# Performance work log

Hardware: AMD Instinct MI355X
Metric: run time of the kernel (lower is better)

Reference implementation:

```python
import jax, jax.numpy as jnp
import numpy as np

N = 50000   # n_nodes
E = 500000  # n_edges
D = 128     # input_dim == hidden_dim
L = 2       # n_layers
K = 5       # Chebyshev filter size


def setup_inputs() -> dict:
    key = jax.random.key(0)
    k0, k1, k2, k3, k4 = jax.random.split(key, 5)
    scale = 1.0 / np.sqrt(D)
    return {
        "edge_index": jax.random.randint(k0, (2, E), 0, N),
        "edge_weight": jax.random.uniform(k1, (E,), dtype=jnp.float32),
        "emb": jax.random.uniform(k2, (N, D), dtype=jnp.float32, minval=-1.0, maxval=1.0),
        "Wx": jax.random.normal(k3, (L, 3, K, D, D), dtype=jnp.float32) * scale,
        "bx": jnp.zeros((L, 3, D), dtype=jnp.float32),
        "Wh": jax.random.normal(k4, (L, 3, K, D, D), dtype=jnp.float32) * scale,
        "bh": jnp.zeros((L, 3, D), dtype=jnp.float32),
    }


def reference(edge_index, edge_weight, emb, Wx, bx, Wh, bh):
    src, dst = edge_index[0], edge_index[1]
    # ChebConv sym-normalized scaled Laplacian with lambda_max=2:
    # L_hat = L - I = -D^{-1/2} A D^{-1/2} (zero diagonal)
    deg = jax.ops.segment_sum(edge_weight, src, num_segments=N)
    dinv = jnp.where(deg > 0, deg ** -0.5, 0.0)
    w = -dinv[src] * edge_weight * dinv[dst]  # [E]

    def prop(x):  # L_hat @ x via gather/scatter over edges
        return jax.ops.segment_sum(w[:, None] * x[src], dst, num_segments=N)

    def cheb(x, W, b):  # sum_k T_k(L_hat) x W_k + b
        Tx0 = x
        out = Tx0 @ W[0]
        Tx1 = prop(Tx0)
        out = out + Tx1 @ W[1]
        for k in range(2, K):
            Tx2 = 2.0 * prop(Tx1) - Tx0
            out = out + Tx2 @ W[k]
            Tx0, Tx1 = Tx1, Tx2
        return out + b

    x = emb
    hidden_states = []
    for l in range(L):
        H = jnp.ones((N, D), x.dtype)  # init__hidd: ones
        Z = jax.nn.sigmoid(cheb(x, Wx[l, 0], bx[l, 0]) + cheb(H, Wh[l, 0], bh[l, 0]))
        R = jax.nn.sigmoid(cheb(x, Wx[l, 1], bx[l, 1]) + cheb(H, Wh[l, 1], bh[l, 1]))
        Ht = jnp.tanh(cheb(x, Wx[l, 2], bx[l, 2]) + cheb(H * R, Wh[l, 2], bh[l, 2]))
        Hn = Z * H + (1.0 - Z) * Ht
        h = jax.nn.relu(Hn)  # dropout is identity in eval mode
        hidden_states.append(h)
        x = h
    return x  # == hidden_states[-1]
```

## Files before the change

kernel.cpp:

```cpp
#include <hip/hip_runtime.h>
#include <math.h>

#define NN 50000
#define EE 500000
#define DD 128
#define KK 5
#define LL 2

typedef _Float16 f16x8 __attribute__((ext_vector_type(8)));
typedef float f32x4 __attribute__((ext_vector_type(4)));

__device__ __forceinline__ ushort f2h(float x) {
    union { _Float16 h; ushort u; } v; v.h = (_Float16)x; return v.u;
}


__global__ __launch_bounds__(256) void edge_pass1(
    const int* __restrict__ src, const int* __restrict__ dst,
    const float* __restrict__ ew,
    float* __restrict__ deg, int* __restrict__ hist)
{
    int e = blockIdx.x * blockDim.x + threadIdx.x;
    if (e >= EE) return;
    atomicAdd(&deg[src[e]], ew[e]);
    atomicAdd(&hist[dst[e]], 1);
}

__global__ __launch_bounds__(256) void dinv_kernel(
    const float* __restrict__ deg, float* __restrict__ dinv)
{
    int i = blockIdx.x * blockDim.x + threadIdx.x;
    if (i >= NN) return;
    float d = deg[i];
    dinv[i] = (d > 0.f) ? (1.f / sqrtf(d)) : 0.f;
}

__global__ __launch_bounds__(1024) void scan_kernel(
    const int* __restrict__ hist, int* __restrict__ row_ptr)
{
    __shared__ int buf[1024];
    __shared__ int carry;
    int tid = threadIdx.x;
    if (tid == 0) { carry = 0; row_ptr[0] = 0; }
    __syncthreads();
    for (int base = 0; base < NN; base += 1024) {
        int i = base + tid;
        int v = (i < NN) ? hist[i] : 0;
        buf[tid] = v;
        __syncthreads();
        for (int off = 1; off < 1024; off <<= 1) {
            int t = (tid >= off) ? buf[tid - off] : 0;
            __syncthreads();
            buf[tid] += t;
            __syncthreads();
        }
        int incl = buf[tid] + carry;
        if (i < NN) row_ptr[i + 1] = incl;
        __syncthreads();
        if (tid == 1023) carry = incl;
        __syncthreads();
    }
}

__global__ __launch_bounds__(256) void copy_fill(
    const int* __restrict__ row_ptr, int* __restrict__ fill)
{
    int i = blockIdx.x * blockDim.x + threadIdx.x;
    if (i < NN) fill[i] = row_ptr[i];
}

__global__ __launch_bounds__(256) void edge_scatter(
    const int* __restrict__ src, const int* __restrict__ dst,
    const float* __restrict__ ew, const float* __restrict__ dinv,
    int* __restrict__ fill,
    int* __restrict__ src_srt, float* __restrict__ w_srt)
{
    int e = blockIdx.x * blockDim.x + threadIdx.x;
    if (e >= EE) return;
    int s = src[e], t = dst[e];
    float w = -dinv[s] * ew[e] * dinv[t];
    int pos = atomicAdd(&fill[t], 1);
    src_srt[pos] = s;
    w_srt[pos] = w;
}

__global__ __launch_bounds__(256) void propv_kernel(
    const int* __restrict__ rp, const int* __restrict__ ss, const float* __restrict__ sw,
    const float* __restrict__ tin, const float* __restrict__ tprev, float* __restrict__ tout,
    float alpha, float beta, int ones_in, int ones_prev)
{
    int i = blockIdx.x * blockDim.x + threadIdx.x;
    if (i >= NN) return;
    float acc = 0.f;
    int e0 = rp[i], e1 = rp[i + 1];
    int e = e0;
    for (; e + 4 <= e1; e += 4) {
        float t0 = ones_in ? 1.f : tin[ss[e]];
        float t1v = ones_in ? 1.f : tin[ss[e + 1]];
        float t2v = ones_in ? 1.f : tin[ss[e + 2]];
        float t3v = ones_in ? 1.f : tin[ss[e + 3]];
        acc += sw[e] * t0 + sw[e + 1] * t1v + sw[e + 2] * t2v + sw[e + 3] * t3v;
    }
    for (; e < e1; ++e) {
        float tv = ones_in ? 1.f : tin[ss[e]];
        acc += sw[e] * tv;
    }
    float pv = ones_prev ? 1.f : (tprev ? tprev[i] : 0.f);
    tout[i] = alpha * acc + beta * pv;
}

__global__ __launch_bounds__(128) void colsum_kernel(
    const float* __restrict__ Wh, float* __restrict__ scol)
{
    int b = blockIdx.x;
    int k = b % KK;
    int g = (b / KK) % 2;
    int l = b / (2 * KK);
    int d = threadIdx.x;
    const float* Wp = Wh + ((size_t)((l * 3 + g) * KK + k)) * DD * DD;
    float s = 0.f;
    for (int r = 0; r < DD; ++r) s += Wp[r * DD + d];
    scol[((size_t)((l * 2 + g) * KK + k)) * DD + d] = s;
}

__global__ __launch_bounds__(256) void wconv_f16(
    const float* __restrict__ W, ushort* __restrict__ out, int mode)
{
    int t = blockIdx.x;
    int st = (mode == 0) ? t : ((t / KK) * 3 + 2) * KK + (t % KK);
    const float* Wp = W + (size_t)st * DD * DD;
    ushort* op = out + (size_t)t * DD * DD;
    for (int idx = threadIdx.x; idx < DD * DD; idx += 256) {
        int rb = idx >> 7, c = idx & 127;
        float w = Wp[c * DD + rb];
        int byte = rb * 256 + (((c * 2) ^ ((rb & 7) << 4)));
        *(ushort*)((char*)op + byte) = f2h(w);
    }
}

__global__ __launch_bounds__(256) void f32_to_f16(
    const float* __restrict__ in, ushort* __restrict__ out, int n8)
{
    int i = blockIdx.x * blockDim.x + threadIdx.x;
    if (i >= n8) return;
    float4 a = ((const float4*)in)[i * 2];
    float4 b = ((const float4*)in)[i * 2 + 1];
    f16x8 o;
    o[0] = (_Float16)a.x; o[1] = (_Float16)a.y; o[2] = (_Float16)a.z; o[3] = (_Float16)a.w;
    o[4] = (_Float16)b.x; o[5] = (_Float16)b.y; o[6] = (_Float16)b.z; o[7] = (_Float16)b.w;
    ((f16x8*)out)[i] = o;
}

__global__ __launch_bounds__(256) void prop_mat(
    const int* __restrict__ rp, const int* __restrict__ ss, const float* __restrict__ sw,
    const ushort* __restrict__ x, const ushort* __restrict__ prev,
    ushort* __restrict__ out, float alpha, float beta)
{
    int node = blockIdx.x * 16 + (threadIdx.x >> 4);
    if (node >= NN) return;
    int lane = threadIdx.x & 15;
    int c = lane * 8;
    float acc[8];
#pragma unroll
    for (int j = 0; j < 8; ++j) acc[j] = 0.f;
    int e0 = rp[node], e1 = rp[node + 1];
    int e = e0;
    for (; e + 4 <= e1; e += 4) {
        int s0 = ss[e], s1 = ss[e + 1], s2 = ss[e + 2], s3 = ss[e + 3];
        float w0 = sw[e], w1 = sw[e + 1], w2 = sw[e + 2], w3 = sw[e + 3];
        f16x8 r0 = *(const f16x8*)(x + (size_t)s0 * DD + c);
        f16x8 r1 = *(const f16x8*)(x + (size_t)s1 * DD + c);
        f16x8 r2 = *(const f16x8*)(x + (size_t)s2 * DD + c);
        f16x8 r3 = *(const f16x8*)(x + (size_t)s3 * DD + c);
#pragma unroll
        for (int j = 0; j < 8; ++j)
            acc[j] += w0 * (float)r0[j] + w1 * (float)r1[j] + w2 * (float)r2[j] + w3 * (float)r3[j];
    }
    for (; e < e1; ++e) {
        int s = ss[e];
        float w = sw[e];
        f16x8 r = *(const f16x8*)(x + (size_t)s * DD + c);
#pragma unroll
        for (int j = 0; j < 8; ++j) acc[j] += w * (float)r[j];
    }
    f16x8 o;
    if (beta != 0.f && prev) {
        f16x8 pv = *(const f16x8*)(prev + (size_t)node * DD + c);
#pragma unroll
        for (int j = 0; j < 8; ++j) o[j] = (_Float16)(alpha * acc[j] + beta * (float)pv[j]);
    } else {
#pragma unroll
        for (int j = 0; j < 8; ++j) o[j] = (_Float16)(alpha * acc[j]);
    }
    *(f16x8*)(out + (size_t)node * DD + c) = o;
}

__global__ __launch_bounds__(256) void cheb_mm_mfma(
    const ushort* __restrict__ T0, const ushort* __restrict__ T1,
    const ushort* __restrict__ T2, const ushort* __restrict__ T3,
    const ushort* __restrict__ T4,
    const ushort* __restrict__ Wt, int gate_stride,
    float* __restrict__ outbase, size_t out_stride, int accumulate, int ngates)
{
    __shared__ ushort Bs[DD * DD];

    const int nwg = gridDim.x;
    const int b = blockIdx.x;
    const int xcd = b & 7, idx = b >> 3;
    const int q = nwg >> 3, rr = nwg & 7;
    const int start = (xcd < rr) ? xcd * (q + 1) : rr * (q + 1) + (xcd - rr) * q;
    const int lin = start + idx;
    const int tile = lin / ngates;
    const int g = lin - tile * ngates;

    const int tid = threadIdx.x;
    const int lane = tid & 63;
    const int wid = tid >> 6;
    const int lr = lane & 15;
    const int lk = lane >> 4;
    const int r0 = tile * 128;
    const ushort* Wg = Wt + (size_t)g * gate_stride;
    const ushort* Ts[5] = {T0, T1, T2, T3, T4};

    f32x4 acc[2][8];
#pragma unroll
    for (int fr = 0; fr < 2; ++fr)
#pragma unroll
        for (int fc = 0; fc < 8; ++fc)
            acc[fr][fc] = (f32x4){0.f, 0.f, 0.f, 0.f};

    int rowg0 = r0 + wid * 32 + lr;
    int rowg1 = rowg0 + 16;
    bool ok0 = rowg0 < NN;
    bool ok1 = rowg1 < NN;

#pragma unroll
    for (int k = 0; k < KK; ++k) {
        const ushort* Tk = Ts[k];
        const ushort* Bg = Wg + (size_t)k * (DD * DD);
        __syncthreads();
#pragma unroll
        for (int i = 0; i < 8; ++i) {
            int off = i * 4096 + tid * 16;
            uint4 v = *(const uint4*)((const char*)Bg + off);
            *(uint4*)((char*)Bs + off) = v;
        }
        f16x8 a[2][4];
#pragma unroll
        for (int fr = 0; fr < 2; ++fr) {
            int rowg = fr ? rowg1 : rowg0;
            bool ok = fr ? ok1 : ok0;
            const ushort* rp2 = Tk + (size_t)rowg * DD + lk * 8;
#pragma unroll
            for (int ko = 0; ko < 4; ++ko) {
                if (ok) a[fr][ko] = *(const f16x8*)(rp2 + ko * 32);
                else a[fr][ko] = (f16x8){0, 0, 0, 0, 0, 0, 0, 0};
            }
        }
        __syncthreads();
#pragma unroll
        for (int ko = 0; ko < 4; ++ko) {
            const int cb = ko * 64 + lk * 16;
#pragma unroll
            for (int fc = 0; fc < 8; ++fc) {
                int rb = fc * 16 + lr;
                int byte = (rb * 256 + cb) ^ ((rb & 7) << 4);
                f16x8 bfrag = *(const f16x8*)((const char*)Bs + byte);
                acc[0][fc] = __builtin_amdgcn_mfma_f32_16x16x32_f16(a[0][ko], bfrag, acc[0][fc], 0, 0, 0);
                acc[1][fc] = __builtin_amdgcn_mfma_f32_16x16x32_f16(a[1][ko], bfrag, acc[1][fc], 0, 0, 0);
            }
        }
    }

    float* outp = outbase + (size_t)g * out_stride;
#pragma unroll
    for (int fr = 0; fr < 2; ++fr) {
#pragma unroll
        for (int j = 0; j < 4; ++j) {
            int grow = r0 + wid * 32 + fr * 16 + lk * 4 + j;
            if (grow < NN) {
#pragma unroll
                for (int fc = 0; fc < 8; ++fc) {
                    int col = fc * 16 + lr;
                    float* p = outp + (size_t)grow * DD + col;
                    float v = acc[fr][fc][j];
                    if (accumulate) *p += v; else *p = v;
                }
            }
        }
    }
}

__global__ __launch_bounds__(256) void gate_zr_kernel(
    float* __restrict__ Xz, float* __restrict__ Xr, ushort* __restrict__ Xr_f16,
    const float* __restrict__ tvec, const float* __restrict__ scol,
    const float* __restrict__ bx, const float* __restrict__ bh, int l)
{
    int idx = blockIdx.x * blockDim.x + threadIdx.x;
    if (idx >= NN * DD) return;
    int i = idx >> 7;
    int d = idx & 127;
    float t1 = tvec[i], t2 = tvec[NN + i], t3 = tvec[2 * NN + i], t4 = tvec[3 * NN + i];

    const float* s0 = scol + (size_t)((l * 2 + 0) * KK) * DD;
    float hz = s0[d] + t1 * s0[DD + d] + t2 * s0[2 * DD + d] + t3 * s0[3 * DD + d] + t4 * s0[4 * DD + d];
    float z = Xz[idx] + bx[(l * 3 + 0) * DD + d] + bh[(l * 3 + 0) * DD + d] + hz;
    Xz[idx] = 1.f / (1.f + expf(-z));

    const float* s1 = scol + (size_t)((l * 2 + 1) * KK) * DD;
    float hr = s1[d] + t1 * s1[DD + d] + t2 * s1[2 * DD + d] + t3 * s1[3 * DD + d] + t4 * s1[4 * DD + d];
    float r = Xr[idx] + bx[(l * 3 + 1) * DD + d] + bh[(l * 3 + 1) * DD + d] + hr;
    float rv = 1.f / (1.f + expf(-r));
    Xr[idx] = rv;
    Xr_f16[idx] = f2h(rv);
}

__global__ __launch_bounds__(256) void gate_final_kernel(
    const float* __restrict__ Xz, const float* __restrict__ Xh,
    const float* __restrict__ bx, const float* __restrict__ bh, int l,
    float* __restrict__ out, ushort* __restrict__ h_f16)
{
    int idx = blockIdx.x * blockDim.x + threadIdx.x;
    if (idx >= NN * DD) return;
    int d = idx & 127;
    float ht = tanhf(Xh[idx] + bx[(l * 3 + 2) * DD + d] + bh[(l * 3 + 2) * DD + d]);
    float z = Xz[idx];
    float hn = z + (1.f - z) * ht;
    float h = hn > 0.f ? hn : 0.f;
    out[idx] = h;
    h_f16[idx] = f2h(h);
}


extern "C" void kernel_launch(void* const* d_in, const int* in_sizes, int n_in,
                              void* d_out, int out_size, void* d_ws, size_t ws_size,
                              hipStream_t stream)
{
    const int*   ei  = (const int*)d_in[0];
    const float* ew  = (const float*)d_in[1];
    const float* emb = (const float*)d_in[2];
    const float* Wx  = (const float*)d_in[3];
    const float* bx  = (const float*)d_in[4];
    const float* Wh  = (const float*)d_in[5];
    const float* bh  = (const float*)d_in[6];
    float* out = (float*)d_out;

    const int* src = ei;
    const int* dst = ei + EE;

    char* ws = (char*)d_ws;
    size_t off = 0;
    auto alloc = [&](size_t nbytes) -> char* {
        char* p = ws + off;
        off = (off + nbytes + 255) & ~(size_t)255;
        return p;
    };
    float*  deg     = (float*)alloc((size_t)NN * 4);
    float*  dinv    = (float*)alloc((size_t)NN * 4);
    int*    hist    = (int*)alloc((size_t)(NN + 1) * 4);
    int*    row_ptr = (int*)alloc((size_t)(NN + 1) * 4);
    int*    fill    = (int*)alloc((size_t)(NN + 1) * 4);
    int*    src_srt = (int*)alloc((size_t)EE * 4);
    float*  w_srt   = (float*)alloc((size_t)EE * 4);
    float*  tvec    = (float*)alloc((size_t)4 * NN * 4);
    float*  scol    = (float*)alloc((size_t)LL * 2 * KK * DD * 4);
    float*  X       = (float*)alloc((size_t)3 * NN * DD * 4);
    ushort* Th      = (ushort*)alloc((size_t)4 * NN * DD * 2);
    ushort* x_f16   = (ushort*)alloc((size_t)NN * DD * 2);
    ushort* Xr_f16  = (ushort*)alloc((size_t)NN * DD * 2);
    ushort* WxT     = (ushort*)alloc((size_t)LL * 3 * KK * DD * DD * 2);
    ushort* WhT2    = (ushort*)alloc((size_t)LL * KK * DD * DD * 2);
    (void)ws_size; (void)in_sizes; (void)n_in; (void)out_size;

    float* Xz = X;
    float* Xr = X + (size_t)NN * DD;
    float* Xh = X + (size_t)2 * NN * DD;
    ushort* T1 = Th;
    ushort* T2 = Th + (size_t)NN * DD;
    ushort* T3 = Th + (size_t)2 * NN * DD;
    ushort* T4 = Th + (size_t)3 * NN * DD;

    const int EG = (EE + 255) / 256;
    const int NG = (NN + 255) / 256;
    const int PG = (NN + 15) / 16;
    const int ELG = (NN * DD + 255) / 256;
    const int MMG = (NN + 127) / 128;
    const int CVG = (NN * DD / 8 + 255) / 256;
    const int GATE_STRIDE = KK * DD * DD;

    hipMemsetAsync(deg, 0, (size_t)NN * 4, stream);
    hipMemsetAsync(hist, 0, (size_t)(NN + 1) * 4, stream);

    edge_pass1<<<EG, 256, 0, stream>>>(src, dst, ew, deg, hist);
    dinv_kernel<<<NG, 256, 0, stream>>>(deg, dinv);
    scan_kernel<<<1, 1024, 0, stream>>>(hist, row_ptr);
    copy_fill<<<NG, 256, 0, stream>>>(row_ptr, fill);
    edge_scatter<<<EG, 256, 0, stream>>>(src, dst, ew, dinv, fill, src_srt, w_srt);

    float* t1 = tvec;
    float* t2 = tvec + NN;
    float* t3 = tvec + 2 * NN;
    float* t4 = tvec + 3 * NN;
    propv_kernel<<<NG, 256, 0, stream>>>(row_ptr, src_srt, w_srt, nullptr, nullptr, t1, 1.f,  0.f, 1, 0);
    propv_kernel<<<NG, 256, 0, stream>>>(row_ptr, src_srt, w_srt, t1, nullptr,      t2, 2.f, -1.f, 0, 1);
    propv_kernel<<<NG, 256, 0, stream>>>(row_ptr, src_srt, w_srt, t2, t1,           t3, 2.f, -1.f, 0, 0);
    propv_kernel<<<NG, 256, 0, stream>>>(row_ptr, src_srt, w_srt, t3, t2,           t4, 2.f, -1.f, 0, 0);

    colsum_kernel<<<LL * 2 * KK, 128, 0, stream>>>(Wh, scol);

    wconv_f16<<<LL * 3 * KK, 256, 0, stream>>>(Wx, WxT, 0);
    wconv_f16<<<LL * KK, 256, 0, stream>>>(Wh, WhT2, 1);

    f32_to_f16<<<CVG, 256, 0, stream>>>(emb, x_f16, NN * DD / 8);

    for (int l = 0; l < LL; ++l) {
        prop_mat<<<PG, 256, 0, stream>>>(row_ptr, src_srt, w_srt, x_f16, nullptr, T1, 1.f,  0.f);
        prop_mat<<<PG, 256, 0, stream>>>(row_ptr, src_srt, w_srt, T1,    x_f16,   T2, 2.f, -1.f);
        prop_mat<<<PG, 256, 0, stream>>>(row_ptr, src_srt, w_srt, T2,    T1,      T3, 2.f, -1.f);
        prop_mat<<<PG, 256, 0, stream>>>(row_ptr, src_srt, w_srt, T3,    T2,      T4, 2.f, -1.f);

        cheb_mm_mfma<<<MMG * 3, 256, 0, stream>>>(x_f16, T1, T2, T3, T4,
                                             WxT + (size_t)l * 3 * GATE_STRIDE, GATE_STRIDE,
                                             Xz, (size_t)NN * DD, 0, 3);

        gate_zr_kernel<<<ELG, 256, 0, stream>>>(Xz, Xr, Xr_f16, tvec, scol, bx, bh, l);

        prop_mat<<<PG, 256, 0, stream>>>(row_ptr, src_srt, w_srt, Xr_f16, nullptr, T1, 1.f,  0.f);
        prop_mat<<<PG, 256, 0, stream>>>(row_ptr, src_srt, w_srt, T1,     Xr_f16,  T2, 2.f, -1.f);
        prop_mat<<<PG, 256, 0, stream>>>(row_ptr, src_srt, w_srt, T2,     T1,      T3, 2.f, -1.f);
        prop_mat<<<PG, 256, 0, stream>>>(row_ptr, src_srt, w_srt, T3,     T2,      T4, 2.f, -1.f);

        cheb_mm_mfma<<<MMG, 256, 0, stream>>>(Xr_f16, T1, T2, T3, T4,
                                             WhT2 + (size_t)l * GATE_STRIDE, 0,
                                             Xh, 0, 1, 1);

        gate_final_kernel<<<ELG, 256, 0, stream>>>(Xz, Xh, bx, bh, l, out, x_f16);
    }
}
```

Baseline: 890.8 us.

## Fuse gate epilogues into Chebyshev MFMA kernels and parallelize row-pointer scan

```diff
diff --git a/kernel.cpp b/kernel.cpp
--- a/kernel.cpp
+++ b/kernel.cpp
@@ -35,30 +35,36 @@
     dinv[i] = (d > 0.f) ? (1.f / sqrtf(d)) : 0.f;
 }
 
+#define SCAN_C ((NN + 1023) / 1024)
 __global__ __launch_bounds__(1024) void scan_kernel(
     const int* __restrict__ hist, int* __restrict__ row_ptr)
 {
-    __shared__ int buf[1024];
-    __shared__ int carry;
-    int tid = threadIdx.x;
-    if (tid == 0) { carry = 0; row_ptr[0] = 0; }
+    __shared__ int sums[1024];
+    const int t = threadIdx.x;
+    const int base = t * SCAN_C;
+    int local[SCAN_C];
+    int s = 0;
+#pragma unroll
+    for (int j = 0; j < SCAN_C; ++j) {
+        int i = base + j;
+        int v = (i < NN) ? hist[i] : 0;
+        s += v;
+        local[j] = s;
+    }
+    sums[t] = s;
     __syncthreads();
-    for (int base = 0; base < NN; base += 1024) {
-        int i = base + tid;
-        int v = (i < NN) ? hist[i] : 0;
-        buf[tid] = v;
+    for (int off = 1; off < 1024; off <<= 1) {
+        int v = (t >= off) ? sums[t - off] : 0;
         __syncthreads();
-        for (int off = 1; off < 1024; off <<= 1) {
-            int t = (tid >= off) ? buf[tid - off] : 0;
-            __syncthreads();
-            buf[tid] += t;
-            __syncthreads();
-        }
-        int incl = buf[tid] + carry;
-        if (i < NN) row_ptr[i + 1] = incl;
+        sums[t] += v;
         __syncthreads();
-        if (tid == 1023) carry = incl;
-        __syncthreads();
+    }
+    int excl = sums[t] - s;
+    if (t == 0) row_ptr[0] = 0;
+#pragma unroll
+    for (int j = 0; j < SCAN_C; ++j) {
+        int i = base + j;
+        if (i < NN) row_ptr[i + 1] = excl + local[j];
     }
 }
 
@@ -195,45 +201,15 @@
     *(f16x8*)(out + (size_t)node * DD + c) = o;
 }
 
-__global__ __launch_bounds__(256) void cheb_mm_mfma(
-    const ushort* __restrict__ T0, const ushort* __restrict__ T1,
-    const ushort* __restrict__ T2, const ushort* __restrict__ T3,
-    const ushort* __restrict__ T4,
-    const ushort* __restrict__ Wt, int gate_stride,
-    float* __restrict__ outbase, size_t out_stride, int accumulate, int ngates)
-{
-    __shared__ ushort Bs[DD * DD];
-
-    const int nwg = gridDim.x;
-    const int b = blockIdx.x;
-    const int xcd = b & 7, idx = b >> 3;
-    const int q = nwg >> 3, rr = nwg & 7;
-    const int start = (xcd < rr) ? xcd * (q + 1) : rr * (q + 1) + (xcd - rr) * q;
-    const int lin = start + idx;
-    const int tile = lin / ngates;
-    const int g = lin - tile * ngates;
-
-    const int tid = threadIdx.x;
-    const int lane = tid & 63;
-    const int wid = tid >> 6;
-    const int lr = lane & 15;
-    const int lk = lane >> 4;
-    const int r0 = tile * 128;
-    const ushort* Wg = Wt + (size_t)g * gate_stride;
-    const ushort* Ts[5] = {T0, T1, T2, T3, T4};
-
-    f32x4 acc[2][8];
+__device__ __forceinline__ void mm_gate(
+    const ushort* __restrict__ const* Ts, const ushort* __restrict__ Wg,
+    ushort* Bs, int rowg0, int rowg1, bool ok0, bool ok1,
+    int tid, int lk, f32x4 acc[2][8], int lr)
+{
 #pragma unroll
     for (int fr = 0; fr < 2; ++fr)
 #pragma unroll
-        for (int fc = 0; fc < 8; ++fc)
-            acc[fr][fc] = (f32x4){0.f, 0.f, 0.f, 0.f};
-
-    int rowg0 = r0 + wid * 32 + lr;
-    int rowg1 = rowg0 + 16;
-    bool ok0 = rowg0 < NN;
-    bool ok1 = rowg1 < NN;
-
+        for (int fc = 0; fc < 8; ++fc) acc[fr][fc] = (f32x4){0.f, 0.f, 0.f, 0.f};
 #pragma unroll
     for (int k = 0; k < KK; ++k) {
         const ushort* Tk = Ts[k];
@@ -250,7 +226,8 @@
         for (int fr = 0; fr < 2; ++fr) {
             int rowg = fr ? rowg1 : rowg0;
             bool ok = fr ? ok1 : ok0;
-            const ushort* rp2 = Tk + (size_t)rowg * DD + lk * 8;
+            const ushort* rp2 = Ts[k] + (size_t)rowg * DD + lk * 8;
+            (void)Tk;
 #pragma unroll
             for (int ko = 0; ko < 4; ++ko) {
                 if (ok) a[fr][ko] = *(const f16x8*)(rp2 + ko * 32);
@@ -271,8 +248,79 @@
             }
         }
     }
-
-    float* outp = outbase + (size_t)g * out_stride;
+}
+
+__device__ __forceinline__ int xcd_swz(int b, int nwg) {
+    int xcd = b & 7, idx = b >> 3;
+    int q = nwg >> 3, rr = nwg & 7;
+    int start = (xcd < rr) ? xcd * (q + 1) : rr * (q + 1) + (xcd - rr) * q;
+    return start + idx;
+}
+
+__global__ __launch_bounds__(256) void cheb_mm_zr(
+    const ushort* __restrict__ T0, const ushort* __restrict__ T1,
+    const ushort* __restrict__ T2, const ushort* __restrict__ T3,
+    const ushort* __restrict__ T4,
+    const ushort* __restrict__ Wt,
+    const float* __restrict__ tvec, const float* __restrict__ scol,
+    const float* __restrict__ bx, const float* __restrict__ bh, int l,
+    float* __restrict__ Xz, ushort* __restrict__ Xr16, float* __restrict__ Xh)
+{
+    __shared__ ushort Bs[DD * DD];
+    const int tile = xcd_swz(blockIdx.x, gridDim.x);
+    const int tid = threadIdx.x;
+    const int lane = tid & 63;
+    const int wid = tid >> 6;
+    const int lr = lane & 15;
+    const int lk = lane >> 4;
+    const int r0 = tile * 128;
+    const ushort* Ts[5] = {T0, T1, T2, T3, T4};
+
+    int rowg0 = r0 + wid * 32 + lr;
+    int rowg1 = rowg0 + 16;
+    bool ok0 = rowg0 < NN;
+    bool ok1 = rowg1 < NN;
+
+    f32x4 accZ[2][8], accB[2][8];
+    mm_gate(Ts, Wt, Bs, rowg0, rowg1, ok0, ok1, tid, lk, accZ, lr);
+    mm_gate(Ts, Wt + (size_t)KK * DD * DD, Bs, rowg0, rowg1, ok0, ok1, tid, lk, accB, lr);
+
+    {
+        const float* s0 = scol + (size_t)((l * 2 + 0) * KK) * DD;
+        const float* s1 = scol + (size_t)((l * 2 + 1) * KK) * DD;
+        const float* bz0 = bx + (size_t)(l * 3 + 0) * DD;
+        const float* bz1 = bh + (size_t)(l * 3 + 0) * DD;
+        const float* br0 = bx + (size_t)(l * 3 + 1) * DD;
+        const float* br1 = bh + (size_t)(l * 3 + 1) * DD;
+#pragma unroll
+        for (int fr = 0; fr < 2; ++fr) {
+#pragma unroll
+            for (int j = 0; j < 4; ++j) {
+                int grow = r0 + wid * 32 + fr * 16 + lk * 4 + j;
+                if (grow < NN) {
+                    float t1 = tvec[grow], t2 = tvec[NN + grow];
+                    float t3 = tvec[2 * NN + grow], t4 = tvec[3 * NN + grow];
+#pragma unroll
+                    for (int fc = 0; fc < 8; ++fc) {
+                        int d = fc * 16 + lr;
+                        size_t idx = (size_t)grow * DD + d;
+                        float hz = s0[d] + t1 * s0[DD + d] + t2 * s0[2 * DD + d]
+                                 + t3 * s0[3 * DD + d] + t4 * s0[4 * DD + d];
+                        float z = accZ[fr][fc][j] + bz0[d] + bz1[d] + hz;
+                        z = 1.f / (1.f + expf(-z));
+                        float hr = s1[d] + t1 * s1[DD + d] + t2 * s1[2 * DD + d]
+                                 + t3 * s1[3 * DD + d] + t4 * s1[4 * DD + d];
+                        float r = accB[fr][fc][j] + br0[d] + br1[d] + hr;
+                        r = 1.f / (1.f + expf(-r));
+                        Xz[idx] = z;
+                        Xr16[idx] = f2h(r);
+                    }
+                }
+            }
+        }
+    }
+
+    mm_gate(Ts, Wt + (size_t)2 * KK * DD * DD, Bs, rowg0, rowg1, ok0, ok1, tid, lk, accZ, lr);
 #pragma unroll
     for (int fr = 0; fr < 2; ++fr) {
 #pragma unroll
@@ -281,54 +329,64 @@
             if (grow < NN) {
 #pragma unroll
                 for (int fc = 0; fc < 8; ++fc) {
-                    int col = fc * 16 + lr;
-                    float* p = outp + (size_t)grow * DD + col;
-                    float v = acc[fr][fc][j];
-                    if (accumulate) *p += v; else *p = v;
+                    int d = fc * 16 + lr;
+                    Xh[(size_t)grow * DD + d] = accZ[fr][fc][j];
                 }
             }
         }
     }
 }
 
-__global__ __launch_bounds__(256) void gate_zr_kernel(
-    float* __restrict__ Xz, float* __restrict__ Xr, ushort* __restrict__ Xr_f16,
-    const float* __restrict__ tvec, const float* __restrict__ scol,
-    const float* __restrict__ bx, const float* __restrict__ bh, int l)
-{
-    int idx = blockIdx.x * blockDim.x + threadIdx.x;
-    if (idx >= NN * DD) return;
-    int i = idx >> 7;
-    int d = idx & 127;
-    float t1 = tvec[i], t2 = tvec[NN + i], t3 = tvec[2 * NN + i], t4 = tvec[3 * NN + i];
-
-    const float* s0 = scol + (size_t)((l * 2 + 0) * KK) * DD;
-    float hz = s0[d] + t1 * s0[DD + d] + t2 * s0[2 * DD + d] + t3 * s0[3 * DD + d] + t4 * s0[4 * DD + d];
-    float z = Xz[idx] + bx[(l * 3 + 0) * DD + d] + bh[(l * 3 + 0) * DD + d] + hz;
-    Xz[idx] = 1.f / (1.f + expf(-z));
-
-    const float* s1 = scol + (size_t)((l * 2 + 1) * KK) * DD;
-    float hr = s1[d] + t1 * s1[DD + d] + t2 * s1[2 * DD + d] + t3 * s1[3 * DD + d] + t4 * s1[4 * DD + d];
-    float r = Xr[idx] + bx[(l * 3 + 1) * DD + d] + bh[(l * 3 + 1) * DD + d] + hr;
-    float rv = 1.f / (1.f + expf(-r));
-    Xr[idx] = rv;
-    Xr_f16[idx] = f2h(rv);
-}
-
-__global__ __launch_bounds__(256) void gate_final_kernel(
-    const float* __restrict__ Xz, const float* __restrict__ Xh,
+__global__ __launch_bounds__(256) void cheb_mm_final(
+    const ushort* __restrict__ T0, const ushort* __restrict__ T1,
+    const ushort* __restrict__ T2, const ushort* __restrict__ T3,
+    const ushort* __restrict__ T4,
+    const ushort* __restrict__ Wt,
+    const float* __restrict__ Xh, const float* __restrict__ Xz,
     const float* __restrict__ bx, const float* __restrict__ bh, int l,
-    float* __restrict__ out, ushort* __restrict__ h_f16)
-{
-    int idx = blockIdx.x * blockDim.x + threadIdx.x;
-    if (idx >= NN * DD) return;
-    int d = idx & 127;
-    float ht = tanhf(Xh[idx] + bx[(l * 3 + 2) * DD + d] + bh[(l * 3 + 2) * DD + d]);
-    float z = Xz[idx];
-    float hn = z + (1.f - z) * ht;
-    float h = hn > 0.f ? hn : 0.f;
-    out[idx] = h;
-    h_f16[idx] = f2h(h);
+    float* __restrict__ out, ushort* __restrict__ h16, int write_f32)
+{
+    __shared__ ushort Bs[DD * DD];
+    const int tile = xcd_swz(blockIdx.x, gridDim.x);
+    const int tid = threadIdx.x;
+    const int lane = tid & 63;
+    const int wid = tid >> 6;
+    const int lr = lane & 15;
+    const int lk = lane >> 4;
+    const int r0 = tile * 128;
+    const ushort* Ts[5] = {T0, T1, T2, T3, T4};
+
+    int rowg0 = r0 + wid * 32 + lr;
+    int rowg1 = rowg0 + 16;
+    bool ok0 = rowg0 < NN;
+    bool ok1 = rowg1 < NN;
+
+    f32x4 acc[2][8];
+    mm_gate(Ts, Wt, Bs, rowg0, rowg1, ok0, ok1, tid, lk, acc, lr);
+
+    const float* b0 = bx + (size_t)(l * 3 + 2) * DD;
+    const float* b1 = bh + (size_t)(l * 3 + 2) * DD;
+#pragma unroll
+    for (int fr = 0; fr < 2; ++fr) {
+#pragma unroll
+        for (int j = 0; j < 4; ++j) {
+            int grow = r0 + wid * 32 + fr * 16 + lk * 4 + j;
+            if (grow < NN) {
+#pragma unroll
+                for (int fc = 0; fc < 8; ++fc) {
+                    int d = fc * 16 + lr;
+                    size_t idx = (size_t)grow * DD + d;
+                    float pre = acc[fr][fc][j] + Xh[idx] + b0[d] + b1[d];
+                    float ht = tanhf(pre);
+                    float z = Xz[idx];
+                    float hn = z + (1.f - z) * ht;
+                    float h = hn > 0.f ? hn : 0.f;
+                    if (write_f32) out[idx] = h;
+                    h16[idx] = f2h(h);
+                }
+            }
+        }
+    }
 }
 
 
@@ -364,7 +422,8 @@
     float*  w_srt   = (float*)alloc((size_t)EE * 4);
     float*  tvec    = (float*)alloc((size_t)4 * NN * 4);
     float*  scol    = (float*)alloc((size_t)LL * 2 * KK * DD * 4);
-    float*  X       = (float*)alloc((size_t)3 * NN * DD * 4);
+    float*  Xz      = (float*)alloc((size_t)NN * DD * 4);
+    float*  Xh      = (float*)alloc((size_t)NN * DD * 4);
     ushort* Th      = (ushort*)alloc((size_t)4 * NN * DD * 2);
     ushort* x_f16   = (ushort*)alloc((size_t)NN * DD * 2);
     ushort* Xr_f16  = (ushort*)alloc((size_t)NN * DD * 2);
@@ -372,9 +431,6 @@
     ushort* WhT2    = (ushort*)alloc((size_t)LL * KK * DD * DD * 2);
     (void)ws_size; (void)in_sizes; (void)n_in; (void)out_size;
 
-    float* Xz = X;
-    float* Xr = X + (size_t)NN * DD;
-    float* Xh = X + (size_t)2 * NN * DD;
     ushort* T1 = Th;
     ushort* T2 = Th + (size_t)NN * DD;
     ushort* T3 = Th + (size_t)2 * NN * DD;
@@ -383,7 +439,6 @@
     const int EG = (EE + 255) / 256;
     const int NG = (NN + 255) / 256;
     const int PG = (NN + 15) / 16;
-    const int ELG = (NN * DD + 255) / 256;
     const int MMG = (NN + 127) / 128;
     const int CVG = (NN * DD / 8 + 255) / 256;
     const int GATE_STRIDE = KK * DD * DD;
@@ -419,21 +474,19 @@
         prop_mat<<<PG, 256, 0, stream>>>(row_ptr, src_srt, w_srt, T2,    T1,      T3, 2.f, -1.f);
         prop_mat<<<PG, 256, 0, stream>>>(row_ptr, src_srt, w_srt, T3,    T2,      T4, 2.f, -1.f);
 
-        cheb_mm_mfma<<<MMG * 3, 256, 0, stream>>>(x_f16, T1, T2, T3, T4,
-                                             WxT + (size_t)l * 3 * GATE_STRIDE, GATE_STRIDE,
-                                             Xz, (size_t)NN * DD, 0, 3);
-
-        gate_zr_kernel<<<ELG, 256, 0, stream>>>(Xz, Xr, Xr_f16, tvec, scol, bx, bh, l);
+        cheb_mm_zr<<<MMG, 256, 0, stream>>>(x_f16, T1, T2, T3, T4,
+                                            WxT + (size_t)l * 3 * GATE_STRIDE,
+                                            tvec, scol, bx, bh, l,
+                                            Xz, Xr_f16, Xh);
 
         prop_mat<<<PG, 256, 0, stream>>>(row_ptr, src_srt, w_srt, Xr_f16, nullptr, T1, 1.f,  0.f);
         prop_mat<<<PG, 256, 0, stream>>>(row_ptr, src_srt, w_srt, T1,     Xr_f16,  T2, 2.f, -1.f);
         prop_mat<<<PG, 256, 0, stream>>>(row_ptr, src_srt, w_srt, T2,     T1,      T3, 2.f, -1.f);
         prop_mat<<<PG, 256, 0, stream>>>(row_ptr, src_srt, w_srt, T3,     T2,      T4, 2.f, -1.f);
 
-        cheb_mm_mfma<<<MMG, 256, 0, stream>>>(Xr_f16, T1, T2, T3, T4,
-                                             WhT2 + (size_t)l * GATE_STRIDE, 0,
-                                             Xh, 0, 1, 1);
-
-        gate_final_kernel<<<ELG, 256, 0, stream>>>(Xz, Xh, bx, bh, l, out, x_f16);
-    }
-}
+        cheb_mm_final<<<MMG, 256, 0, stream>>>(Xr_f16, T1, T2, T3, T4,
+                                               WhT2 + (size_t)l * GATE_STRIDE,
+                                               Xh, Xz, bx, bh, l,
+                                               out, x_f16, (l == LL - 1) ? 1 : 0);
+    }
+}
```

New measurement: 957.5 us. 7.5% more time.
